# Optimization experiments

Hardware: AMD Instinct MI355X
Metric: run time of the kernel (lower is better)

Reference implementation:

```python
import jax, jax.numpy as jnp
import numpy as np

D_MODEL = 1024
D_STATE = 16
D_CONV = 4
EXPAND = 2
D_INNER = EXPAND * D_MODEL  # 2048
B, L = 2, 2048


def setup_inputs() -> dict:
    key = jax.random.key(0)
    ks = jax.random.split(key, 8)
    s = lambda k, shape, scale: jax.random.normal(k, shape, jnp.float32) * scale
    x = jax.random.normal(ks[0], (B, L, D_MODEL), jnp.float32)
    W_in = s(ks[1], (D_MODEL, 2 * D_INNER), D_MODEL ** -0.5)      # in_proj.weight.T
    conv_w = s(ks[2], (D_INNER, 1, D_CONV), D_CONV ** -0.5)        # depthwise conv kernel (O,I/g,K)
    conv_b = s(ks[3], (D_INNER,), 0.02)
    W_x = s(ks[4], (D_INNER, 2 * D_STATE), D_INNER ** -0.5)        # x_proj.weight.T
    W_dt = s(ks[5], (D_STATE, D_INNER), D_STATE ** -0.5)           # dt_proj.weight.T
    b_dt = s(ks[6], (D_INNER,), 0.02)
    A_log = jnp.log(jnp.broadcast_to(
        jnp.arange(1, D_STATE + 1, dtype=jnp.float32), (D_INNER, D_STATE)))
    D_param = jnp.ones((D_INNER,), jnp.float32)
    W_out = s(ks[7], (D_INNER, D_MODEL), D_INNER ** -0.5)          # out_proj.weight.T
    return dict(x=x, W_in=W_in, conv_w=conv_w, conv_b=conv_b, W_x=W_x,
                W_dt=W_dt, b_dt=b_dt, A_log=A_log, D=D_param, W_out=W_out)


def _s6_forward(x, W_in, conv_w, conv_b, W_x, W_dt, b_dt, A_log, D, W_out):
    silu = jax.nn.silu
    # input projection and gate split
    xz = x @ W_in                                   # (B,L,2*d_inner)
    xc, z = jnp.split(xz, 2, axis=-1)               # each (B,L,d_inner)
    # causal depthwise conv1d (torch pads d_conv-1 both sides then truncates to L
    # == left-pad d_conv-1 only)
    xc_t = jnp.transpose(xc, (0, 2, 1))             # (B,d_inner,L)
    xc_t = jax.lax.conv_general_dilated(
        xc_t, conv_w, window_strides=(1,), padding=[(D_CONV - 1, 0)],
        dimension_numbers=('NCH', 'OIH', 'NCH'),
        feature_group_count=D_INNER) + conv_b[None, :, None]
    xs = silu(jnp.transpose(xc_t, (0, 2, 1)))       # (B,L,d_inner)
    # SSM parameterization
    dBC = xs @ W_x                                  # (B,L,2*d_state)
    d_raw, Bm = jnp.split(dBC, 2, axis=-1)          # (B,L,d_state) each
    C = Bm                                          # C = B as in source
    delta = jax.nn.softplus(d_raw @ W_dt + b_dt)    # (B,L,d_inner)
    A = -jnp.exp(A_log)                             # (d_inner,d_state)
    dA = jnp.exp(delta[..., None] * A)              # (B,L,d_inner,d_state)
    dBu = delta[..., None] * Bm[:, :, None, :] * xs[..., None]  # (B,L,n,d)
    # inclusive associative scan: h_t = dA_t * h_{t-1} + dBu_t
    def comb(e1, e2):
        a1, b1 = e1
        a2, b2 = e2
        return a2 * a1, a2 * b1 + b2
    _, h = jax.lax.associative_scan(comb, (dA, dBu), axis=1)
    y = jnp.einsum('blnd,bld->bln', h, C) + D * xs  # (B,L,d_inner)
    y = y * silu(z)
    return y @ W_out                                # (B,L,d_model)


def reference(x, W_in, conv_w, conv_b, W_x, W_dt, b_dt, A_log, D, W_out):
    return _s6_forward(x, W_in, conv_w, conv_b, W_x, W_dt, b_dt, A_log, D, W_out)
```

## Files before the change

kernel.cpp:

```cpp
#include <hip/hip_runtime.h>
#include <hip/hip_bf16.h>
#include <math.h>

#define DMODEL 1024
#define DSTATE 16
#define DCONV  4
#define DINNER 2048
#define BB     2
#define LL     2048
#define MROWS  (BB*LL)
#define NXZ    (2*DINNER)
#define NC     64
#define CL     32
#define GK2    4
#define KC2    (DINNER/GK2)
#define CPKS   4
#define CPKC   (DINNER/CPKS)

typedef __attribute__((ext_vector_type(8))) short bf16x8;
typedef __attribute__((ext_vector_type(4))) float f32x4;

#define GLD_LDS16(g, l) __builtin_amdgcn_global_load_lds( \
    (const __attribute__((address_space(1))) void*)(g),   \
    (__attribute__((address_space(3))) void*)(l), 16, 0, 0)

__device__ __forceinline__ float softplus_fast(float x) {
    return fmaxf(x, 0.f) + __logf(1.f + __expf(-fabsf(x)));
}
__device__ __forceinline__ float sigmoid_fast(float x) {
    return __builtin_amdgcn_rcpf(1.f + __expf(-x));
}
__device__ __forceinline__ float bf2f(unsigned short u) {
    union { float f; unsigned int i; } v; v.i = ((unsigned int)u) << 16; return v.f;
}
__device__ __forceinline__ unsigned short f2bf(float f) {
    union { __hip_bfloat16 h; unsigned short u; } v;
    v.h = __float2bfloat16(f);
    return v.u;
}

__device__ __forceinline__ void transpose_body(const float* __restrict__ W,
                                               __hip_bfloat16* __restrict__ Wt,
                                               int K, int N, int bx, int by, int tid) {
    __shared__ __hip_bfloat16 tile[32][33];
    int n0 = bx * 32, k0 = by * 32;
    int tx = tid & 31, ty = tid >> 5;
    #pragma unroll
    for (int j = 0; j < 4; ++j)
        tile[ty + j * 8][tx] = __float2bfloat16(W[(size_t)(k0 + ty + j * 8) * N + n0 + tx]);
    __syncthreads();
    #pragma unroll
    for (int j = 0; j < 4; ++j)
        Wt[(size_t)(n0 + ty + j * 8) * K + k0 + tx] = tile[tx][ty + j * 8];
}

__global__ __launch_bounds__(256) void prep_kernel(const float* __restrict__ x,
                                                   const float* __restrict__ W_in,
                                                   const float* __restrict__ W_out,
                                                   __hip_bfloat16* __restrict__ xb,
                                                   __hip_bfloat16* __restrict__ W_in_t,
                                                   __hip_bfloat16* __restrict__ W_out_t) {
    int id = blockIdx.x, tid = threadIdx.x;
    if (id < 4096) {
        int i = id * 256 + tid;
        float4 v = *(const float4*)(x + (size_t)i * 4);
        ushort4 u = { f2bf(v.x), f2bf(v.y), f2bf(v.z), f2bf(v.w) };
        *(ushort4*)((unsigned short*)xb + (size_t)i * 4) = u;
    } else if (id < 8192) {
        int bid = id - 4096;
        transpose_body(W_in, W_in_t, DMODEL, NXZ, bid & 127, bid >> 7, tid);
    } else {
        int bid = id - 8192;
        transpose_body(W_out, W_out_t, DINNER, DMODEL, bid & 31, bid >> 5, tid);
    }
}

#define BARRIER() asm volatile("s_barrier" ::: "memory")
#define WAIT_LGKM0() do { asm volatile("s_waitcnt lgkmcnt(0)" ::: "memory"); \
                          __builtin_amdgcn_sched_barrier(0); } while (0)

#define READ_A(DST, MH)                                                     \
    _Pragma("unroll")                                                       \
    for (int m = 0; m < 4; ++m) {                                           \
        int ar = arb + (MH) * 64 + m * 16;                                  \
        DST[m][0] = *(const bf16x8*)(lA + ar * 64 + so0);                   \
        DST[m][1] = *(const bf16x8*)(lA + ar * 64 + so1);                   \
    }
#define READ_B(DST, NH)                                                     \
    _Pragma("unroll")                                                       \
    for (int n = 0; n < 2; ++n) {                                           \
        int br = brb + (NH) * 32 + n * 16;                                  \
        DST[n][0] = *(const bf16x8*)(lB + br * 64 + so0);                   \
        DST[n][1] = *(const bf16x8*)(lB + br * 64 + so1);                   \
    }
#define MFMA_Q(AF, BF, MO, NO)                                              \
    _Pragma("unroll")                                                       \
    for (int m = 0; m < 4; ++m)                                             \
        _Pragma("unroll")                                                   \
        for (int n = 0; n < 2; ++n) {                                       \
            acc[(MO) + m][(NO) + n] = __builtin_amdgcn_mfma_f32_16x16x32_bf16( \
                AF[m][0], BF[n][0], acc[(MO) + m][(NO) + n], 0, 0, 0);      \
            acc[(MO) + m][(NO) + n] = __builtin_amdgcn_mfma_f32_16x16x32_bf16( \
                AF[m][1], BF[n][1], acc[(MO) + m][(NO) + n], 0, 0, 0);      \
        }

__global__ __launch_bounds__(512, 2) void gemm_bt_8ph(const __hip_bfloat16* __restrict__ A,
                                                      const __hip_bfloat16* __restrict__ Bt,
                                                      __hip_bfloat16* __restrict__ C,
                                                      int M, int N, int K) {
    extern __shared__ __hip_bfloat16 sm[];
    const int tid  = threadIdx.x;
    const int lane = tid & 63;
    const int wid  = tid >> 6;
    const int wm   = wid >> 2;
    const int wn   = wid & 3;
    const int lr   = lane & 15;
    const int kg   = lane >> 4;
    const int fid = blockIdx.y * gridDim.x + blockIdx.x;
    const int cpx = (gridDim.x * gridDim.y) >> 3;
    const int swz = (fid & 7) * cpx + (fid >> 3);
    const int row0 = (swz / gridDim.x) * 256;
    const int col0 = (swz % gridDim.x) * 256;
    const int NT   = K >> 6;

    int su[2], sr[2], sk[2];
    #pragma unroll
    for (int c = 0; c < 2; ++c) {
        su[c] = c * 512 + tid;
        sr[c] = su[c] >> 3;
        sk[c] = ((su[c] & 7) ^ (sr[c] & 7)) << 3;
    }
    auto STAGE = [&](int tt, int mat, int half) {
        if (tt >= NT) return;
        const __hip_bfloat16* src = mat ? Bt : A;
        int base0 = mat ? col0 : row0;
        __hip_bfloat16* dst = sm + (((tt & 1) * 2 + mat) * 16384) + half * 8192;
        int k0t = tt << 6;
        #pragma unroll
        for (int c = 0; c < 2; ++c)
            GLD_LDS16(src + (size_t)(base0 + half * 128 + sr[c]) * K + k0t + sk[c],
                      dst + su[c] * 8);
    };

    f32x4 acc[8][4];
    #pragma unroll
    for (int m = 0; m < 8; ++m)
        #pragma unroll
        for (int n = 0; n < 4; ++n)
            acc[m][n] = (f32x4){0.f, 0.f, 0.f, 0.f};

    const int arb = wm * 128 + lr;
    const int brb = wn * 64 + lr;
    const int so0 = ((kg)     ^ (lr & 7)) << 3;
    const int so1 = ((kg + 4) ^ (lr & 7)) << 3;

    STAGE(0, 0, 0); STAGE(0, 0, 1); STAGE(0, 1, 0); STAGE(0, 1, 1);
    STAGE(1, 0, 0); STAGE(1, 1, 0);
    asm volatile("s_waitcnt vmcnt(4)" ::: "memory");
    BARRIER();

    bf16x8 a0[4][2], a1[4][2], b0[2][2], b1[2][2];
    for (int t = 0; t < NT; ++t) {
        const __hip_bfloat16* lA = sm + ((t & 1) * 2) * 16384;
        const __hip_bfloat16* lB = lA + 16384;
        READ_A(a0, 0); READ_B(b0, 0);
        STAGE(t + 1, 0, 1);
        BARRIER(); WAIT_LGKM0();
        __builtin_amdgcn_s_setprio(1); MFMA_Q(a0, b0, 0, 0); __builtin_amdgcn_s_setprio(0);
        BARRIER();
        READ_A(a1, 1);
        STAGE(t + 1, 1, 1);
        BARRIER(); WAIT_LGKM0();
        __builtin_amdgcn_s_setprio(1); MFMA_Q(a1, b0, 4, 0); __builtin_amdgcn_s_setprio(0);
        BARRIER();
        READ_B(b1, 1);
        STAGE(t + 2, 0, 0);
        BARRIER(); WAIT_LGKM0();
        __builtin_amdgcn_s_setprio(1); MFMA_Q(a0, b1, 0, 2); __builtin_amdgcn_s_setprio(0);
        BARRIER();
        STAGE(t + 2, 1, 0);
        BARRIER(); WAIT_LGKM0();
        __builtin_amdgcn_s_setprio(1); MFMA_Q(a1, b1, 4, 2); __builtin_amdgcn_s_setprio(0);
        asm volatile("s_waitcnt vmcnt(4)" ::: "memory");
        BARRIER();
    }

    #pragma unroll
    for (int m = 0; m < 8; ++m)
        #pragma unroll
        for (int n = 0; n < 4; ++n)
            #pragma unroll
            for (int r = 0; r < 4; ++r)
                C[(size_t)(row0 + wm * 128 + m * 16 + kg * 4 + r) * N
                  + col0 + wn * 64 + n * 16 + lr] = __float2bfloat16(acc[m][n][r]);
}

__global__ __launch_bounds__(256) void gemm_bt_splitk(const __hip_bfloat16* __restrict__ A,
                                                      const __hip_bfloat16* __restrict__ Bt,
                                                      float* __restrict__ part,
                                                      int M, int N, int Kc, int LD) {
    __shared__ __hip_bfloat16 lA[128 * 32];
    __shared__ __hip_bfloat16 lB[128 * 32];
    const int tid  = threadIdx.x;
    const int lane = tid & 63;
    const int wid  = tid >> 6;
    const int row0 = blockIdx.y * 128;
    const int col0 = blockIdx.x * 128;
    const int kOff = blockIdx.z * Kc;
    float* C = part + (size_t)blockIdx.z * M * N;
    const int wr = (wid >> 1) * 64;
    const int wc = (wid & 1) * 64;
    const int lr = lane & 15;
    const int kg = lane >> 4;

    f32x4 acc[4][4];
    #pragma unroll
    for (int m = 0; m < 4; ++m)
        #pragma unroll
        for (int n = 0; n < 4; ++n)
            acc[m][n] = (f32x4){0.f, 0.f, 0.f, 0.f};

    for (int k0 = 0; k0 < Kc; k0 += 32) {
        #pragma unroll
        for (int c = 0; c < 2; ++c) {
            int chunk = wid * 2 + c;
            int idx = chunk * 64 + lane;
            int r = idx >> 2, q = idx & 3;
            GLD_LDS16(A  + (size_t)(row0 + r) * LD + kOff + k0 + q * 8, lA + chunk * 512);
            GLD_LDS16(Bt + (size_t)(col0 + r) * LD + kOff + k0 + q * 8, lB + chunk * 512);
        }
        __syncthreads();
        bf16x8 af[4], bv[4];
        #pragma unroll
        for (int m = 0; m < 4; ++m)
            af[m] = *reinterpret_cast<const bf16x8*>(lA + (wr + m * 16 + lr) * 32 + kg * 8);
        #pragma unroll
        for (int n = 0; n < 4; ++n)
            bv[n] = *reinterpret_cast<const bf16x8*>(lB + (wc + n * 16 + lr) * 32 + kg * 8);
        #pragma unroll
        for (int m = 0; m < 4; ++m)
            #pragma unroll
            for (int n = 0; n < 4; ++n)
                acc[m][n] = __builtin_amdgcn_mfma_f32_16x16x32_bf16(af[m], bv[n], acc[m][n], 0, 0, 0);
        __syncthreads();
    }
    #pragma unroll
    for (int m = 0; m < 4; ++m)
        #pragma unroll
        for (int n = 0; n < 4; ++n)
            #pragma unroll
            for (int r = 0; r < 4; ++r)
                C[(size_t)(row0 + wr + m * 16 + kg * 4 + r) * N + col0 + wc + n * 16 + lr] = acc[m][n][r];
}

__global__ __launch_bounds__(256) void splitk_reduce_kernel(const float* __restrict__ part,
                                                            float* __restrict__ out) {
    size_t i = (size_t)blockIdx.x * 256 + threadIdx.x;
    const float4* p = (const float4*)part;
    const size_t MN4 = (size_t)MROWS * DMODEL / 4;
    float4 s0 = p[i], s1 = p[MN4 + i], s2 = p[2 * MN4 + i], s3 = p[3 * MN4 + i];
    float4 r;
    r.x = (s0.x + s1.x) + (s2.x + s3.x);
    r.y = (s0.y + s1.y) + (s2.y + s3.y);
    r.z = (s0.z + s1.z) + (s2.z + s3.z);
    r.w = (s0.w + s1.w) + (s2.w + s3.w);
    ((float4*)out)[i] = r;
}

__global__ __launch_bounds__(256) void convproj_kernel(const __hip_bfloat16* __restrict__ xzb,
                                                       const float* __restrict__ conv_w,
                                                       const float* __restrict__ conv_b,
                                                       const float* __restrict__ W_x,
                                                       __hip_bfloat16* __restrict__ xsb,
                                                       float* __restrict__ dBCp) {
    __shared__ unsigned short lxs[8][CPKC + 8];
    __shared__ float4 lp[4][8][8];
    const int tid  = threadIdx.x;
    const int row0 = blockIdx.x * 8;
    const int ksl  = blockIdx.y;
    const int d0   = ksl * CPKC;

    #pragma unroll
    for (int j = 0; j < 4; ++j) {
        int q  = tid + j * 256;
        int r  = q >> 7;
        int dq = q & 127;
        int d  = d0 + dq * 4;
        int row = row0 + r;
        int l   = row & (LL - 1);
        float4 w0 = *(const float4*)(conv_w + (d + 0) * 4);
        float4 w1 = *(const float4*)(conv_w + (d + 1) * 4);
        float4 w2 = *(const float4*)(conv_w + (d + 2) * 4);
        float4 w3 = *(const float4*)(conv_w + (d + 3) * 4);
        float4 s  = *(const float4*)(conv_b + d);
        #pragma unroll
        for (int tt = 0; tt < 4; ++tt) {
            if (l - 3 + tt >= 0) {
                ushort4 uv = *(const ushort4*)((const unsigned short*)xzb
                                               + (size_t)(row - 3 + tt) * NXZ + d);
                s.x += (&w0.x)[tt] * bf2f(uv.x);
                s.y += (&w1.x)[tt] * bf2f(uv.y);
                s.z += (&w2.x)[tt] * bf2f(uv.z);
                s.w += (&w3.x)[tt] * bf2f(uv.w);
            }
        }
        s.x *= sigmoid_fast(s.x); s.y *= sigmoid_fast(s.y);
        s.z *= sigmoid_fast(s.z); s.w *= sigmoid_fast(s.w);
        ushort4 o = { f2bf(s.x), f2bf(s.y), f2bf(s.z), f2bf(s.w) };
        *(ushort4*)&lxs[r][dq * 4] = o;
        *(ushort4*)((unsigned short*)xsb + (size_t)row * DINNER + d) = o;
    }
    __syncthreads();

    const int ks2 = tid >> 6;
    const int r   = (tid >> 3) & 7;
    const int nb  = tid & 7;
    const int kl0 = ks2 * 128;
    const float* wp = W_x + (size_t)(d0 + kl0) * 32 + nb * 4;
    float4 acc = {0.f, 0.f, 0.f, 0.f};
    #pragma unroll 2
    for (int k4 = 0; k4 < 32; ++k4) {
        ushort4 uv = *(const ushort4*)&lxs[r][kl0 + k4 * 4];
        float x0 = bf2f(uv.x), x1 = bf2f(uv.y), x2 = bf2f(uv.z), x3 = bf2f(uv.w);
        float4 wv0 = *(const float4*)(wp + (k4 * 4 + 0) * 32);
        float4 wv1 = *(const float4*)(wp + (k4 * 4 + 1) * 32);
        float4 wv2 = *(const float4*)(wp + (k4 * 4 + 2) * 32);
        float4 wv3 = *(const float4*)(wp + (k4 * 4 + 3) * 32);
        acc.x += x0 * wv0.x + x1 * wv1.x + x2 * wv2.x + x3 * wv3.x;
        acc.y += x0 * wv0.y + x1 * wv1.y + x2 * wv2.y + x3 * wv3.y;
        acc.z += x0 * wv0.z + x1 * wv1.z + x2 * wv2.z + x3 * wv3.z;
        acc.w += x0 * wv0.w + x1 * wv1.w + x2 * wv2.w + x3 * wv3.w;
    }
    lp[ks2][r][nb] = acc;
    __syncthreads();
    if (ks2 == 0) {
        float4 p0 = lp[0][r][nb], p1 = lp[1][r][nb], p2 = lp[2][r][nb], p3 = lp[3][r][nb];
        float4 s;
        s.x = (p0.x + p1.x) + (p2.x + p3.x);
        s.y = (p0.y + p1.y) + (p2.y + p3.y);
        s.z = (p0.z + p1.z) + (p2.z + p3.z);
        s.w = (p0.w + p1.w) + (p2.w + p3.w);
        *(float4*)(dBCp + ((size_t)ksl * MROWS + row0 + r) * 32 + nb * 4) = s;
    }
}

__global__ __launch_bounds__(256) void xreduce_kernel(const float* __restrict__ dBCp,
                                                      float* __restrict__ dBC) {
    int i = blockIdx.x * 256 + threadIdx.x;
    float s0 = dBCp[i];
    float s1 = dBCp[(size_t)MROWS * 32 + i];
    float s2 = dBCp[2 * (size_t)MROWS * 32 + i];
    float s3 = dBCp[3 * (size_t)MROWS * 32 + i];
    dBC[i] = (s0 + s1) + (s2 + s3);
}

__global__ __launch_bounds__(256, 2) void scanA_kernel(const __hip_bfloat16* __restrict__ xsb,
                                                       const float* __restrict__ dBC,
                                                       const float* __restrict__ W_dt,
                                                       const float* __restrict__ b_dt,
                                                       float* __restrict__ aProd,
                                                       float* __restrict__ hEnd) {
    int t = blockIdx.x * 256 + threadIdx.x;
    int d = t & (DINNER - 1);
    int c = (t >> 11) & (NC - 1);
    int b = t >> 17;
    float Wd[DSTATE], h[DSTATE];
    #pragma unroll
    for (int k = 0; k < DSTATE; ++k) Wd[k] = W_dt[k * DINNER + d];
    float bd = b_dt[d];
    float dsum = 0.f;
    #pragma unroll
    for (int n = 0; n < DSTATE; ++n) h[n] = 0.f;

    for (int i = 0; i < CL; ++i) {
        size_t row = (size_t)b * LL + c * CL + i;
        const float4* qp = (const float4*)(dBC + row * 32);
        float4 r0 = qp[0], r1 = qp[1], r2 = qp[2], r3 = qp[3];
        float dacc = bd
            + r0.x * Wd[0]  + r0.y * Wd[1]  + r0.z * Wd[2]  + r0.w * Wd[3]
            + r1.x * Wd[4]  + r1.y * Wd[5]  + r1.z * Wd[6]  + r1.w * Wd[7]
            + r2.x * Wd[8]  + r2.y * Wd[9]  + r2.z * Wd[10] + r2.w * Wd[11]
            + r3.x * Wd[12] + r3.y * Wd[13] + r3.z * Wd[14] + r3.w * Wd[15];
        float delta = softplus_fast(dacc);
        dsum += delta;
        float xv = bf2f(((const unsigned short*)xsb)[row * DINNER + d]);
        float dx = delta * xv;
        float ex = __expf(-delta);
        float4 r4 = qp[4], r5 = qp[5], r6 = qp[6], r7 = qp[7];
        float a = ex;
        h[0]  = a * h[0]  + dx * r4.x; a *= ex;
        h[1]  = a * h[1]  + dx * r4.y; a *= ex;
        h[2]  = a * h[2]  + dx * r4.z; a *= ex;
        h[3]  = a * h[3]  + dx * r4.w; a *= ex;
        h[4]  = a * h[4]  + dx * r5.x; a *= ex;
        h[5]  = a * h[5]  + dx * r5.y; a *= ex;
        h[6]  = a * h[6]  + dx * r5.z; a *= ex;
        h[7]  = a * h[7]  + dx * r5.w; a *= ex;
        h[8]  = a * h[8]  + dx * r6.x; a *= ex;
        h[9]  = a * h[9]  + dx * r6.y; a *= ex;
        h[10] = a * h[10] + dx * r6.z; a *= ex;
        h[11] = a * h[11] + dx * r6.w; a *= ex;
        h[12] = a * h[12] + dx * r7.x; a *= ex;
        h[13] = a * h[13] + dx * r7.y; a *= ex;
        h[14] = a * h[14] + dx * r7.z; a *= ex;
        h[15] = a * h[15] + dx * r7.w;
    }
    size_t obase = ((size_t)((b * NC + c) * DSTATE)) * DINNER + d;
    float exs = __expf(-dsum);
    float ap = exs;
    #pragma unroll
    for (int n = 0; n < DSTATE; ++n) {
        aProd[obase + (size_t)n * DINNER] = ap;
        hEnd [obase + (size_t)n * DINNER] = h[n];
        ap *= exs;
    }
}

__global__ __launch_bounds__(256) void scanB_kernel(const float* __restrict__ aProd,
                                                    float* __restrict__ hEnd) {
    int t = blockIdx.x * 256 + threadIdx.x;
    int d = t & (DINNER - 1);
    int n = (t >> 11) & (DSTATE - 1);
    int b = t >> 15;
    float cur = 0.f;
    for (int c = 0; c < NC; ++c) {
        size_t idx = ((size_t)((b * NC + c) * DSTATE + n)) * DINNER + d;
        float a  = aProd[idx];
        float hh = hEnd[idx];
        hEnd[idx] = cur;
        cur = a * cur + hh;
    }
}

__global__ __launch_bounds__(256, 2) void scanC_kernel(const __hip_bfloat16* __restrict__ xzb,
                                                       const __hip_bfloat16* __restrict__ xsb,
                                                       const float* __restrict__ dBC,
                                                       const float* __restrict__ W_dt,
                                                       const float* __restrict__ b_dt,
                                                       const float* __restrict__ Dp,
                                                       const float* __restrict__ hEnd,
                                                       __hip_bfloat16* __restrict__ ygb) {
    int t = blockIdx.x * 256 + threadIdx.x;
    int d = t & (DINNER - 1);
    int c = (t >> 11) & (NC - 1);
    int b = t >> 17;
    float Wd[DSTATE], h[DSTATE];
    #pragma unroll
    for (int k = 0; k < DSTATE; ++k) Wd[k] = W_dt[k * DINNER + d];
    float bd = b_dt[d];
    float Dd = Dp[d];
    size_t obase = ((size_t)((b * NC + c) * DSTATE)) * DINNER + d;
    #pragma unroll
    for (int n = 0; n < DSTATE; ++n) h[n] = hEnd[obase + (size_t)n * DINNER];

    for (int i = 0; i < CL; ++i) {
        size_t row = (size_t)b * LL + c * CL + i;
        const float4* qp = (const float4*)(dBC + row * 32);
        float4 r0 = qp[0], r1 = qp[1], r2 = qp[2], r3 = qp[3];
        float dacc = bd
            + r0.x * Wd[0]  + r0.y * Wd[1]  + r0.z * Wd[2]  + r0.w * Wd[3]
            + r1.x * Wd[4]  + r1.y * Wd[5]  + r1.z * Wd[6]  + r1.w * Wd[7]
            + r2.x * Wd[8]  + r2.y * Wd[9]  + r2.z * Wd[10] + r2.w * Wd[11]
            + r3.x * Wd[12] + r3.y * Wd[13] + r3.z * Wd[14] + r3.w * Wd[15];
        float delta = softplus_fast(dacc);
        float xv = bf2f(((const unsigned short*)xsb)[row * DINNER + d]);
        float dx = delta * xv;
        float ex = __expf(-delta);
        float4 r4 = qp[4], r5 = qp[5], r6 = qp[6], r7 = qp[7];
        float a = ex, p = 0.f;
        h[0]  = a * h[0]  + dx * r4.x; p += h[0]  * r4.x; a *= ex;
        h[1]  = a * h[1]  + dx * r4.y; p += h[1]  * r4.y; a *= ex;
        h[2]  = a * h[2]  + dx * r4.z; p += h[2]  * r4.z; a *= ex;
        h[3]  = a * h[3]  + dx * r4.w; p += h[3]  * r4.w; a *= ex;
        h[4]  = a * h[4]  + dx * r5.x; p += h[4]  * r5.x; a *= ex;
        h[5]  = a * h[5]  + dx * r5.y; p += h[5]  * r5.y; a *= ex;
        h[6]  = a * h[6]  + dx * r5.z; p += h[6]  * r5.z; a *= ex;
        h[7]  = a * h[7]  + dx * r5.w; p += h[7]  * r5.w; a *= ex;
        h[8]  = a * h[8]  + dx * r6.x; p += h[8]  * r6.x; a *= ex;
        h[9]  = a * h[9]  + dx * r6.y; p += h[9]  * r6.y; a *= ex;
        h[10] = a * h[10] + dx * r6.z; p += h[10] * r6.z; a *= ex;
        h[11] = a * h[11] + dx * r6.w; p += h[11] * r6.w; a *= ex;
        h[12] = a * h[12] + dx * r7.x; p += h[12] * r7.x; a *= ex;
        h[13] = a * h[13] + dx * r7.y; p += h[13] * r7.y; a *= ex;
        h[14] = a * h[14] + dx * r7.z; p += h[14] * r7.z; a *= ex;
        h[15] = a * h[15] + dx * r7.w; p += h[15] * r7.w;
        float y = p + Dd * xv;
        float zv = bf2f(((const unsigned short*)xzb)[row * NXZ + DINNER + d]);
        float sz = zv * sigmoid_fast(zv);
        ygb[row * DINNER + d] = __float2bfloat16(y * sz);
    }
}

extern "C" void kernel_launch(void* const* d_in, const int* in_sizes, int n_in,
                              void* d_out, int out_size, void* d_ws, size_t ws_size,
                              hipStream_t stream) {
    const float* x      = (const float*)d_in[0];
    const float* W_in   = (const float*)d_in[1];
    const float* conv_w = (const float*)d_in[2];
    const float* conv_b = (const float*)d_in[3];
    const float* W_x    = (const float*)d_in[4];
    const float* W_dt   = (const float*)d_in[5];
    const float* b_dt   = (const float*)d_in[6];
    const float* Dp     = (const float*)d_in[8];
    const float* W_out  = (const float*)d_in[9];
    float* out = (float*)d_out;

    float* ws = (float*)d_ws;
    float* region0 = ws;
    __hip_bfloat16* xzb = (__hip_bfloat16*)region0;
    float* g2part = region0;
    float* xs_    = region0 + (size_t)16777216;
    __hip_bfloat16* xsb = (__hip_bfloat16*)xs_;
    float* dBC    = xs_ + (size_t)4194304;
    float* dBCp   = dBC + (size_t)131072;
    float* aProd  = dBCp + (size_t)524288;
    float* hEnd   = aProd + (size_t)4194304;
    float* wott   = hEnd + (size_t)4194304;
    float* alias  = wott + (size_t)1048576;
    __hip_bfloat16* xb      = (__hip_bfloat16*)alias;
    __hip_bfloat16* W_in_t  = xb + (size_t)MROWS * DMODEL;
    __hip_bfloat16* ygb     = (__hip_bfloat16*)alias;
    __hip_bfloat16* W_out_t = (__hip_bfloat16*)wott;

    (void)hipFuncSetAttribute(reinterpret_cast<const void*>(gemm_bt_8ph),
                              hipFuncAttributeMaxDynamicSharedMemorySize, 131072);

    prep_kernel<<<10240, 256, 0, stream>>>(x, W_in, W_out, xb, W_in_t, W_out_t);
    gemm_bt_8ph<<<dim3(NXZ / 256, MROWS / 256), 512, 131072, stream>>>(xb, W_in_t, xzb, MROWS, NXZ, DMODEL);
    convproj_kernel<<<dim3(MROWS / 8, CPKS), 256, 0, stream>>>(xzb, conv_w, conv_b, W_x, xsb, dBCp);
    xreduce_kernel<<<(MROWS * 32) / 256, 256, 0, stream>>>(dBCp, dBC);
    scanA_kernel<<<(BB * NC * DINNER) / 256, 256, 0, stream>>>(xsb, dBC, W_dt, b_dt, aProd, hEnd);
    scanB_kernel<<<(BB * DSTATE * DINNER) / 256, 256, 0, stream>>>(aProd, hEnd);
    scanC_kernel<<<(BB * NC * DINNER) / 256, 256, 0, stream>>>(xzb, xsb, dBC, W_dt, b_dt, Dp, hEnd, ygb);
    gemm_bt_splitk<<<dim3(DMODEL / 128, MROWS / 128, GK2), 256, 0, stream>>>(ygb, W_out_t, g2part,
                                                                             MROWS, DMODEL, KC2, DINNER);
    splitk_reduce_kernel<<<(MROWS * DMODEL / 4) / 256, 256, 0, stream>>>(g2part, out);
}
```

Before: 223.6 us.

## Store split-K GEMM partials in bf16 and double convproj K-splits

The output projection's split-K partial sums are now written and read as bf16 instead of fp32, halving the traffic through the partial buffer and the reduction kernel. Separately, the conv+x_proj kernel splits the inner dimension into 8 slices instead of 4, doubling the grid and halving per-block work. The xreduce kernel is generalized to sum CPKS slices, and the workspace layout is adjusted to fit the larger partial buffer. Rounding partials to bf16 before the sum adds numerical error, and the extra slices add reduction traffic.

```diff
diff --git a/kernel.cpp b/kernel.cpp
--- a/kernel.cpp
+++ b/kernel.cpp
@@ -14,7 +14,7 @@
 #define CL     32
 #define GK2    4
 #define KC2    (DINNER/GK2)
-#define CPKS   4
+#define CPKS   8
 #define CPKC   (DINNER/CPKS)
 
 typedef __attribute__((ext_vector_type(8))) short bf16x8;
@@ -197,7 +197,7 @@
 
 __global__ __launch_bounds__(256) void gemm_bt_splitk(const __hip_bfloat16* __restrict__ A,
                                                       const __hip_bfloat16* __restrict__ Bt,
-                                                      float* __restrict__ part,
+                                                      __hip_bfloat16* __restrict__ part,
                                                       int M, int N, int Kc, int LD) {
     __shared__ __hip_bfloat16 lA[128 * 32];
     __shared__ __hip_bfloat16 lB[128 * 32];
@@ -207,7 +207,7 @@
     const int row0 = blockIdx.y * 128;
     const int col0 = blockIdx.x * 128;
     const int kOff = blockIdx.z * Kc;
-    float* C = part + (size_t)blockIdx.z * M * N;
+    __hip_bfloat16* C = part + (size_t)blockIdx.z * M * N;
     const int wr = (wid >> 1) * 64;
     const int wc = (wid & 1) * 64;
     const int lr = lane & 15;
@@ -250,20 +250,24 @@
         for (int n = 0; n < 4; ++n)
             #pragma unroll
             for (int r = 0; r < 4; ++r)
-                C[(size_t)(row0 + wr + m * 16 + kg * 4 + r) * N + col0 + wc + n * 16 + lr] = acc[m][n][r];
-}
-
-__global__ __launch_bounds__(256) void splitk_reduce_kernel(const float* __restrict__ part,
+                C[(size_t)(row0 + wr + m * 16 + kg * 4 + r) * N + col0 + wc + n * 16 + lr] =
+                    __float2bfloat16(acc[m][n][r]);
+}
+
+__global__ __launch_bounds__(256) void splitk_reduce_kernel(const __hip_bfloat16* __restrict__ part,
                                                             float* __restrict__ out) {
     size_t i = (size_t)blockIdx.x * 256 + threadIdx.x;
-    const float4* p = (const float4*)part;
-    const size_t MN4 = (size_t)MROWS * DMODEL / 4;
-    float4 s0 = p[i], s1 = p[MN4 + i], s2 = p[2 * MN4 + i], s3 = p[3 * MN4 + i];
+    const unsigned short* p = (const unsigned short*)part;
+    const size_t MN = (size_t)MROWS * DMODEL;
+    ushort4 a0 = *(const ushort4*)(p + i * 4);
+    ushort4 a1 = *(const ushort4*)(p + MN + i * 4);
+    ushort4 a2 = *(const ushort4*)(p + 2 * MN + i * 4);
+    ushort4 a3 = *(const ushort4*)(p + 3 * MN + i * 4);
     float4 r;
-    r.x = (s0.x + s1.x) + (s2.x + s3.x);
-    r.y = (s0.y + s1.y) + (s2.y + s3.y);
-    r.z = (s0.z + s1.z) + (s2.z + s3.z);
-    r.w = (s0.w + s1.w) + (s2.w + s3.w);
+    r.x = (bf2f(a0.x) + bf2f(a1.x)) + (bf2f(a2.x) + bf2f(a3.x));
+    r.y = (bf2f(a0.y) + bf2f(a1.y)) + (bf2f(a2.y) + bf2f(a3.y));
+    r.z = (bf2f(a0.z) + bf2f(a1.z)) + (bf2f(a2.z) + bf2f(a3.z));
+    r.w = (bf2f(a0.w) + bf2f(a1.w)) + (bf2f(a2.w) + bf2f(a3.w));
     ((float4*)out)[i] = r;
 }
 
@@ -281,10 +285,10 @@
     const int d0   = ksl * CPKC;
 
     #pragma unroll
-    for (int j = 0; j < 4; ++j) {
+    for (int j = 0; j < 2; ++j) {
         int q  = tid + j * 256;
-        int r  = q >> 7;
-        int dq = q & 127;
+        int r  = q >> 6;
+        int dq = q & 63;
         int d  = d0 + dq * 4;
         int row = row0 + r;
         int l   = row & (LL - 1);
@@ -315,11 +319,11 @@
     const int ks2 = tid >> 6;
     const int r   = (tid >> 3) & 7;
     const int nb  = tid & 7;
-    const int kl0 = ks2 * 128;
+    const int kl0 = ks2 * (CPKC / 4);
     const float* wp = W_x + (size_t)(d0 + kl0) * 32 + nb * 4;
     float4 acc = {0.f, 0.f, 0.f, 0.f};
     #pragma unroll 2
-    for (int k4 = 0; k4 < 32; ++k4) {
+    for (int k4 = 0; k4 < CPKC / 16; ++k4) {
         ushort4 uv = *(const ushort4*)&lxs[r][kl0 + k4 * 4];
         float x0 = bf2f(uv.x), x1 = bf2f(uv.y), x2 = bf2f(uv.z), x3 = bf2f(uv.w);
         float4 wv0 = *(const float4*)(wp + (k4 * 4 + 0) * 32);
@@ -347,11 +351,11 @@
 __global__ __launch_bounds__(256) void xreduce_kernel(const float* __restrict__ dBCp,
                                                       float* __restrict__ dBC) {
     int i = blockIdx.x * 256 + threadIdx.x;
-    float s0 = dBCp[i];
-    float s1 = dBCp[(size_t)MROWS * 32 + i];
-    float s2 = dBCp[2 * (size_t)MROWS * 32 + i];
-    float s3 = dBCp[3 * (size_t)MROWS * 32 + i];
-    dBC[i] = (s0 + s1) + (s2 + s3);
+    float s = 0.f;
+    #pragma unroll
+    for (int ks = 0; ks < CPKS; ++ks)
+        s += dBCp[(size_t)ks * MROWS * 32 + i];
+    dBC[i] = s;
 }
 
 __global__ __launch_bounds__(256, 2) void scanA_kernel(const __hip_bfloat16* __restrict__ xsb,
@@ -508,12 +512,12 @@
     float* ws = (float*)d_ws;
     float* region0 = ws;
     __hip_bfloat16* xzb = (__hip_bfloat16*)region0;
-    float* g2part = region0;
+    __hip_bfloat16* g2part = (__hip_bfloat16*)region0;
     float* xs_    = region0 + (size_t)16777216;
     __hip_bfloat16* xsb = (__hip_bfloat16*)xs_;
     float* dBC    = xs_ + (size_t)4194304;
     float* dBCp   = dBC + (size_t)131072;
-    float* aProd  = dBCp + (size_t)524288;
+    float* aProd  = dBCp + (size_t)1048576;
     float* hEnd   = aProd + (size_t)4194304;
     float* wott   = hEnd + (size_t)4194304;
     float* alias  = wott + (size_t)1048576;
```

New measurement: 220.6 us. No clear change (-1.4%).
